# Kernel tuning notes

Hardware: AMD Instinct MI355X
Metric: run time of the kernel (lower is better)

Reference implementation:

```python
import jax, jax.numpy as jnp
import numpy as np

B, T, E, H = 8, 2048, 1024, 128

def setup_inputs() -> dict:
    key = jax.random.key(0)
    k1, k2, k3, k4 = jax.random.split(key, 4)
    s = 0.02
    return {
        "x":  jax.random.normal(k1, (B, T, E), dtype=jnp.float32),
        "Wq": jax.random.normal(k2, (E, H), dtype=jnp.float32) * s,
        "Wk": jax.random.normal(k3, (E, H), dtype=jnp.float32) * s,
        "Wv": jax.random.normal(k4, (E, H), dtype=jnp.float32) * s,
    }

def reference(x, Wq, Wk, Wv):
    # q,k,v: [B,T,H]
    q = jnp.einsum("bte,eh->bth", x, Wq)
    k = jnp.einsum("bte,eh->bth", x, Wk)
    v = jnp.einsum("bte,eh->bth", x, Wv)
    scale = jnp.asarray(q.shape[-1], q.dtype) ** -0.5
    wei = jnp.einsum("bqh,bkh->bqk", q, k) * scale  # [B,T,T]
    causal = jnp.tril(jnp.ones((wei.shape[1], wei.shape[2]), dtype=bool))
    wei = jnp.where(causal, wei, jnp.asarray(-jnp.inf, wei.dtype))
    wei = jax.nn.softmax(wei, axis=-1)
    # dropout_prob = 0.0 -> identity
    return jnp.einsum("bqk,bkh->bqh", wei, v)
```

## Files before the change

### kernel.cpp

```cpp
#include <hip/hip_runtime.h>

#define BB 8
#define TT 2048
#define EE 1024
#define HH 128

typedef __bf16 bf16;
typedef __attribute__((ext_vector_type(8))) __bf16 bf16x8;
typedef __attribute__((ext_vector_type(4))) __bf16 bf16x4;
typedef __attribute__((ext_vector_type(4))) float f32x4;
typedef __attribute__((ext_vector_type(16))) float f32x16;

__device__ __host__ inline int qb_off(int qb) {
  int h = qb >> 1;
  return qb + h * (h - 1) + ((qb & 1) ? h : 0);
}
#define NSLAB 72

__device__ inline void gload_lds16(const bf16* g, bf16* l) {
  __builtin_amdgcn_global_load_lds((const __attribute__((address_space(1))) unsigned int*)g,
                                   (__attribute__((address_space(3))) unsigned int*)l,
                                   16, 0, 0);
}

__global__ __launch_bounds__(256) void prep_kernel(const float* __restrict__ x,
                                                   bf16* __restrict__ xb,
                                                   const float* __restrict__ wq,
                                                   const float* __restrict__ wk,
                                                   const float* __restrict__ wv,
                                                   bf16* __restrict__ wt) {
  __shared__ float tile[64][65];
  const int bid = blockIdx.x;
  if (bid < 4096) {
    const size_t base = (size_t)bid * 4096 + threadIdx.x * 4;
#pragma unroll
    for (int j = 0; j < 4; ++j) {
      size_t idx = base + j * 1024;
      f32x4 xv = *(const f32x4*)(x + idx);
      bf16x4 xo;
#pragma unroll
      for (int i = 0; i < 4; ++i) xo[i] = (bf16)xv[i];
      *(bf16x4*)(xb + idx) = xo;
    }
  } else {
    const int id = bid - 4096;
    const int z = id >> 5;
    const int h0 = ((id >> 4) & 1) * 64;
    const int k0 = (id & 15) * 64;
    const float* w = (z == 0) ? wq : ((z == 1) ? wk : wv);
    const int c = threadIdx.x & 63;
    const int r0 = threadIdx.x >> 6;
#pragma unroll
    for (int i = 0; i < 16; ++i) {
      int tt = r0 + i * 4;
      tile[tt][c] = w[(size_t)(k0 + tt) * HH + h0 + c];
    }
    __syncthreads();
#pragma unroll
    for (int i = 0; i < 16; ++i) {
      int hh = r0 + i * 4;
      wt[((size_t)(z * HH + h0 + hh)) * EE + k0 + c] = (bf16)tile[c][hh];
    }
  }
}

__global__ __launch_bounds__(256) void gemm_kernel(const bf16* __restrict__ xb,
                                                   const bf16* __restrict__ wt,
                                                   bf16* __restrict__ q,
                                                   bf16* __restrict__ k,
                                                   bf16* __restrict__ vt) {
  __shared__ bf16 As[2][128 * 32];
  __shared__ bf16 Bs[2][96 * 32];
  const int tid = threadIdx.x;
  const int lane = tid & 63;
  const int wave = tid >> 6;
  const int l16 = lane & 15;
  const int quad = lane >> 4;
  const int wm = wave & 1;
  const int wn = wave >> 1;
  const int bm = blockIdx.x;
  const int ntile = blockIdx.y;

  const int trow = tid >> 2;
  const int tsub = (tid & 3) * 8;
  const bf16* gA = xb + (size_t)(bm * 128 + trow) * EE + tsub;
  const bf16* gB = wt + (size_t)(ntile * 96 + trow) * EE + tsub;

  f32x4 acc[4][3];
#pragma unroll
  for (int rg = 0; rg < 4; ++rg)
#pragma unroll
    for (int nt = 0; nt < 3; ++nt) acc[rg][nt] = f32x4{0.f, 0.f, 0.f, 0.f};

  auto stage = [&](int bufi, int ks) {
    gload_lds16(gA + ks * 32, &As[bufi][wave * 512]);
    gload_lds16(gA + (size_t)64 * EE + ks * 32, &As[bufi][2048 + wave * 512]);
    gload_lds16(gB + ks * 32, &Bs[bufi][wave * 512]);
    if (tid < 128)
      gload_lds16(gB + (size_t)64 * EE + ks * 32, &Bs[bufi][2048 + wave * 512]);
  };

  stage(0, 0);
  __syncthreads();

  int buf = 0;
  for (int ks = 0; ks < EE / 32; ++ks) {
    if (ks < EE / 32 - 1) stage(buf ^ 1, ks + 1);

    bf16x8 af[4], bf_[3];
#pragma unroll
    for (int rg = 0; rg < 4; ++rg)
      af[rg] = *(const bf16x8*)&As[buf][(wm * 64 + rg * 16 + l16) * 32 + quad * 8];
#pragma unroll
    for (int nt = 0; nt < 3; ++nt)
      bf_[nt] = *(const bf16x8*)&Bs[buf][(wn * 48 + nt * 16 + l16) * 32 + quad * 8];
#pragma unroll
    for (int rg = 0; rg < 4; ++rg)
#pragma unroll
      for (int nt = 0; nt < 3; ++nt)
        acc[rg][nt] = __builtin_amdgcn_mfma_f32_16x16x32_bf16(af[rg], bf_[nt], acc[rg][nt], 0, 0, 0);

    __syncthreads();
    buf ^= 1;
  }

#pragma unroll
  for (int rg = 0; rg < 4; ++rg)
#pragma unroll
    for (int nt = 0; nt < 3; ++nt) {
      int col = ntile * 96 + wn * 48 + nt * 16 + l16;
      int z = col >> 7;
      int n = col & 127;
      int row0 = bm * 128 + wm * 64 + rg * 16 + quad * 4;
      if (z == 2) {
        int bb = row0 >> 11;
        int t0 = row0 & (TT - 1);
        bf16x4 pkv;
#pragma unroll
        for (int r = 0; r < 4; ++r) pkv[r] = (bf16)acc[rg][nt][r];
        *(bf16x4*)&vt[((size_t)(bb * HH + n)) * TT + t0] = pkv;
      } else {
        bf16* op = (z == 0) ? q : k;
#pragma unroll
        for (int r = 0; r < 4; ++r)
          op[(size_t)(row0 + r) * HH + n] = (bf16)acc[rg][nt][r];
      }
    }
}

__device__ __forceinline__ unsigned pk2(float a, float b) {
  union { __bf16 h[2]; unsigned u; } x;
  x.h[0] = (__bf16)a;
  x.h[1] = (__bf16)b;
  return x.u;
}

__device__ __forceinline__ void plswap(unsigned& a, unsigned& b) {
  asm volatile("v_permlane32_swap_b32 %0, %1" : "+v"(a), "+v"(b));
}

__global__ __launch_bounds__(256, 2) void flash_kernel(const bf16* __restrict__ q,
                                                       const bf16* __restrict__ k,
                                                       const bf16* __restrict__ vt,
                                                       bf16* __restrict__ opart,
                                                       float* __restrict__ lpart) {
  __shared__ bf16 Ks[2][64 * 128];
  __shared__ bf16 Vs[128 * 64];

  const int b = blockIdx.x & 7;
  int j = (NSLAB - 1) - (blockIdx.x >> 3);
  int qb = 0, ns = 1;
  while (j >= ns) { j -= ns; ++qb; ns = ((2 * qb + 1) >> 2) + 1; }
  const int s = j;
  const int kt0 = s * 4;
  const int kt1 = min(kt0 + 3, 2 * qb + 1);

  const int tid = threadIdx.x;
  const int lane = tid & 63;
  const int wave = tid >> 6;
  const int l32 = lane & 31;
  const int hi = lane >> 5;
  const int qrow = qb * 128 + wave * 32 + l32;
  const int kdiag = qb * 4 + wave;

  bf16x8 qf[8];
  {
    const bf16* qp = q + (size_t)(b * TT + qrow) * HH + hi * 8;
#pragma unroll
    for (int h16 = 0; h16 < 8; ++h16) qf[h16] = *(const bf16x8*)(qp + h16 * 16);
  }

  f32x16 O[4];
#pragma unroll
  for (int ht = 0; ht < 4; ++ht)
#pragma unroll
    for (int r = 0; r < 16; ++r) O[ht][r] = 0.f;
  float L = 0.f;

  const int krow_s = tid >> 4;
  const int kchk_s = (tid & 15) ^ (krow_s & 7);
  const int vrow_s = tid >> 3;
  const int vchk_s = (tid & 7) ^ (vrow_s & 7);
  const bf16* kg = k + (size_t)b * TT * HH;
  const bf16* vg = vt + (size_t)b * HH * TT;

  auto stageK = [&](int bufi, int kt) {
#pragma unroll
    for (int i = 0; i < 4; ++i)
      gload_lds16(kg + (size_t)(kt * 64 + i * 16 + krow_s) * HH + kchk_s * 8,
                  &Ks[bufi][(i * 256 + wave * 64) * 8]);
  };
  auto stageV = [&](int kt) {
#pragma unroll
    for (int i = 0; i < 4; ++i)
      gload_lds16(vg + (size_t)(i * 32 + vrow_s) * TT + kt * 64 + vchk_s * 8,
                  &Vs[(i * 256 + wave * 64) * 8]);
  };

  const int kxor = (l32 & 7) << 3;
  const float c_ = 0.12753257680406733f;

  stageK(0, kt0);
  stageV(kt0);
  __syncthreads();

  int buf = 0;
  for (int kt = kt0; kt <= kt1; ++kt) {
    if (kt < kt1) stageK(buf ^ 1, kt + 1);

#pragma unroll
    for (int khalf = 0; khalf < 2; ++khalf) {
      const int k32 = kt * 2 + khalf;
      if (k32 <= kdiag) {
        const bf16* kls = &Ks[buf][(khalf * 32 + l32) * 128];
        bf16x8 kf[8];
#pragma unroll
        for (int h16 = 0; h16 < 8; ++h16)
          kf[h16] = *(const bf16x8*)&kls[(h16 * 16 + hi * 8) ^ kxor];

        f32x16 S;
#pragma unroll
        for (int r = 0; r < 16; ++r) S[r] = 0.f;
        __builtin_amdgcn_s_setprio(1);
#pragma unroll
        for (int h16 = 0; h16 < 8; ++h16)
          S = __builtin_amdgcn_mfma_f32_32x32x16_bf16(kf[h16], qf[h16], S, 0, 0, 0);
        __builtin_amdgcn_s_setprio(0);

        float p[16];
        if (k32 == kdiag) {
          const int kkb = k32 * 32 + 4 * hi;
#pragma unroll
          for (int r = 0; r < 16; ++r) {
            int kk = kkb + (r & 3) + 8 * (r >> 2);
            p[r] = (kk <= qrow) ? exp2f(S[r] * c_) : 0.f;
          }
        } else {
#pragma unroll
          for (int r = 0; r < 16; ++r) p[r] = exp2f(S[r] * c_);
        }
        L += (((p[0] + p[1]) + (p[2] + p[3])) + ((p[4] + p[5]) + (p[6] + p[7]))) +
             (((p[8] + p[9]) + (p[10] + p[11])) + ((p[12] + p[13]) + (p[14] + p[15])));

#pragma unroll
        for (int s16 = 0; s16 < 2; ++s16) {
          unsigned w0 = pk2(p[s16 * 8 + 0], p[s16 * 8 + 1]);
          unsigned w1 = pk2(p[s16 * 8 + 2], p[s16 * 8 + 3]);
          unsigned w2 = pk2(p[s16 * 8 + 4], p[s16 * 8 + 5]);
          unsigned w3 = pk2(p[s16 * 8 + 6], p[s16 * 8 + 7]);
          plswap(w0, w2);
          plswap(w1, w3);
          union { unsigned u[4]; bf16x8 v; } af;
          af.u[0] = w0;
          af.u[1] = w1;
          af.u[2] = w2;
          af.u[3] = w3;
          bf16x8 vf[4];
#pragma unroll
          for (int ht = 0; ht < 4; ++ht)
            vf[ht] = *(const bf16x8*)&Vs[(l32 + 32 * ht) * 64 +
                                         ((khalf * 32 + s16 * 16 + hi * 8) ^ kxor)];
          __builtin_amdgcn_s_setprio(1);
#pragma unroll
          for (int ht = 0; ht < 4; ++ht)
            O[ht] = __builtin_amdgcn_mfma_f32_32x32x16_bf16(af.v, vf[ht], O[ht], 0, 0, 0);
          __builtin_amdgcn_s_setprio(0);
        }
      }
    }
    __syncthreads();
    if (kt < kt1) {
      stageV(kt + 1);
      __syncthreads();
    }
    buf ^= 1;
  }

  L += __shfl_xor(L, 32, 64);

  const size_t slab = (size_t)(b * NSLAB + qb_off(qb) + s);
  bf16* op = opart + slab * (128 * 128) + (size_t)wave * 32 * 128;
#pragma unroll
  for (int ht = 0; ht < 4; ++ht)
#pragma unroll
    for (int r = 0; r < 16; ++r) {
      int qr = (r & 3) + 8 * (r >> 2) + 4 * hi;
      op[qr * 128 + ht * 32 + l32] = (bf16)O[ht][r];
    }
  if (hi == 0) lpart[slab * 128 + wave * 32 + l32] = L;
}

__global__ __launch_bounds__(128) void combine_kernel(const bf16* __restrict__ opart,
                                                      const float* __restrict__ lpart,
                                                      float* __restrict__ out) {
  const int b = blockIdx.x;
  const int qt16 = blockIdx.y;
  const int half = blockIdx.z;
  const int row = threadIdx.x >> 3;
  const int colo = (threadIdx.x & 7) * 8 + half * 64;
  const int qb = qt16 >> 3;
  const int srow = (qt16 & 7) * 16 + row;
  const int ns = ((2 * qb + 1) >> 2) + 1;
  const size_t slab0 = (size_t)(b * NSLAB + qb_off(qb));

  float acc[8];
#pragma unroll
  for (int j = 0; j < 8; ++j) acc[j] = 0.f;
  float L = 0.f;

  int s = 0;
  for (; s + 4 <= ns; s += 4) {
    float l0 = lpart[(slab0 + s + 0) * 128 + srow];
    float l1 = lpart[(slab0 + s + 1) * 128 + srow];
    float l2 = lpart[(slab0 + s + 2) * 128 + srow];
    float l3 = lpart[(slab0 + s + 3) * 128 + srow];
    bf16x8 v0 = *(const bf16x8*)(opart + (slab0 + s + 0) * (128 * 128) + srow * 128 + colo);
    bf16x8 v1 = *(const bf16x8*)(opart + (slab0 + s + 1) * (128 * 128) + srow * 128 + colo);
    bf16x8 v2 = *(const bf16x8*)(opart + (slab0 + s + 2) * (128 * 128) + srow * 128 + colo);
    bf16x8 v3 = *(const bf16x8*)(opart + (slab0 + s + 3) * (128 * 128) + srow * 128 + colo);
    L += (l0 + l1) + (l2 + l3);
#pragma unroll
    for (int j = 0; j < 8; ++j)
      acc[j] += ((float)v0[j] + (float)v1[j]) + ((float)v2[j] + (float)v3[j]);
  }
  for (; s < ns; ++s) {
    L += lpart[(slab0 + s) * 128 + srow];
    bf16x8 ov = *(const bf16x8*)(opart + (slab0 + s) * (128 * 128) + srow * 128 + colo);
#pragma unroll
    for (int j = 0; j < 8; ++j) acc[j] += (float)ov[j];
  }
  float invL = 1.f / L;
  float* o = out + ((size_t)(b * TT + qt16 * 16 + row)) * HH + colo;
  f32x4 o0, o1;
#pragma unroll
  for (int j = 0; j < 4; ++j) { o0[j] = acc[j] * invL; o1[j] = acc[j + 4] * invL; }
  *(f32x4*)o = o0;
  *(f32x4*)(o + 4) = o1;
}

extern "C" void kernel_launch(void* const* d_in, const int* in_sizes, int n_in,
                              void* d_out, int out_size, void* d_ws, size_t ws_size,
                              hipStream_t stream) {
  const float* x = (const float*)d_in[0];
  const float* wq = (const float*)d_in[1];
  const float* wk = (const float*)d_in[2];
  const float* wv = (const float*)d_in[3];
  float* out = (float*)d_out;

  char* ws = (char*)d_ws;
  const size_t NE = (size_t)BB * TT * HH;
  bf16* wt = (bf16*)ws;
  bf16* xb = (bf16*)(ws + (1 << 20));
  bf16* q = (bf16*)(ws + (33 << 20));
  bf16* k = q + NE;
  bf16* vt = k + NE;
  bf16* opart = xb;
  float* lpart = (float*)(opart + (size_t)(BB * NSLAB) * 128 * 128);

  prep_kernel<<<dim3(4192), 256, 0, stream>>>(x, xb, wq, wk, wv, wt);
  gemm_kernel<<<dim3(128, 4), 256, 0, stream>>>(xb, wt, q, k, vt);
  flash_kernel<<<dim3(576), 256, 0, stream>>>(q, k, vt, opart, lpart);
  combine_kernel<<<dim3(8, 128, 2), 128, 0, stream>>>(opart, lpart, out);
}
```

Before: 153.9 us.

## Fuse fp32-to-bf16 conversion of x into the projection GEMM A-tile loads

The separate prep pass that converted all of x to a bf16 workspace copy is removed. The GEMM now reads fp32 x directly into registers, converts it to bf16, and writes it into the LDS A buffer with software prefetch one k-step ahead. The weight transpose stays in its own small kernel, and the workspace layout is compacted. This drops a full read and write pass over x, but each x tile is now read in fp32 by four column-tile blocks, and the A operand no longer uses async global-to-LDS loads, which raises register use and the cost of the GEMM main loop.

```diff
diff --git a/kernel.cpp b/kernel.cpp
--- a/kernel.cpp
+++ b/kernel.cpp
@@ -23,48 +23,31 @@
                                    16, 0, 0);
 }
 
-__global__ __launch_bounds__(256) void prep_kernel(const float* __restrict__ x,
-                                                   bf16* __restrict__ xb,
-                                                   const float* __restrict__ wq,
-                                                   const float* __restrict__ wk,
-                                                   const float* __restrict__ wv,
-                                                   bf16* __restrict__ wt) {
+__global__ __launch_bounds__(256) void wt_kernel(const float* __restrict__ wq,
+                                                 const float* __restrict__ wk,
+                                                 const float* __restrict__ wv,
+                                                 bf16* __restrict__ wt) {
   __shared__ float tile[64][65];
-  const int bid = blockIdx.x;
-  if (bid < 4096) {
-    const size_t base = (size_t)bid * 4096 + threadIdx.x * 4;
-#pragma unroll
-    for (int j = 0; j < 4; ++j) {
-      size_t idx = base + j * 1024;
-      f32x4 xv = *(const f32x4*)(x + idx);
-      bf16x4 xo;
-#pragma unroll
-      for (int i = 0; i < 4; ++i) xo[i] = (bf16)xv[i];
-      *(bf16x4*)(xb + idx) = xo;
-    }
-  } else {
-    const int id = bid - 4096;
-    const int z = id >> 5;
-    const int h0 = ((id >> 4) & 1) * 64;
-    const int k0 = (id & 15) * 64;
-    const float* w = (z == 0) ? wq : ((z == 1) ? wk : wv);
-    const int c = threadIdx.x & 63;
-    const int r0 = threadIdx.x >> 6;
-#pragma unroll
-    for (int i = 0; i < 16; ++i) {
-      int tt = r0 + i * 4;
-      tile[tt][c] = w[(size_t)(k0 + tt) * HH + h0 + c];
-    }
-    __syncthreads();
-#pragma unroll
-    for (int i = 0; i < 16; ++i) {
-      int hh = r0 + i * 4;
-      wt[((size_t)(z * HH + h0 + hh)) * EE + k0 + c] = (bf16)tile[c][hh];
-    }
-  }
-}
-
-__global__ __launch_bounds__(256) void gemm_kernel(const bf16* __restrict__ xb,
+  const int z = blockIdx.z;
+  const float* w = (z == 0) ? wq : ((z == 1) ? wk : wv);
+  const int k0 = blockIdx.x * 64;
+  const int h0 = blockIdx.y * 64;
+  const int c = threadIdx.x & 63;
+  const int r0 = threadIdx.x >> 6;
+#pragma unroll
+  for (int i = 0; i < 16; ++i) {
+    int tt = r0 + i * 4;
+    tile[tt][c] = w[(size_t)(k0 + tt) * HH + h0 + c];
+  }
+  __syncthreads();
+#pragma unroll
+  for (int i = 0; i < 16; ++i) {
+    int hh = r0 + i * 4;
+    wt[((size_t)(z * HH + h0 + hh)) * EE + k0 + c] = (bf16)tile[c][hh];
+  }
+}
+
+__global__ __launch_bounds__(256) void gemm_kernel(const float* __restrict__ x,
                                                    const bf16* __restrict__ wt,
                                                    bf16* __restrict__ q,
                                                    bf16* __restrict__ k,
@@ -83,8 +66,9 @@
 
   const int trow = tid >> 2;
   const int tsub = (tid & 3) * 8;
-  const bf16* gA = xb + (size_t)(bm * 128 + trow) * EE + tsub;
+  const float* gA = x + (size_t)(bm * 128 + trow) * EE + tsub;
   const bf16* gB = wt + (size_t)(ntile * 96 + trow) * EE + tsub;
+  const int awr = trow * 32 + tsub;
 
   f32x4 acc[4][3];
 #pragma unroll
@@ -92,21 +76,31 @@
 #pragma unroll
     for (int nt = 0; nt < 3; ++nt) acc[rg][nt] = f32x4{0.f, 0.f, 0.f, 0.f};
 
-  auto stage = [&](int bufi, int ks) {
-    gload_lds16(gA + ks * 32, &As[bufi][wave * 512]);
-    gload_lds16(gA + (size_t)64 * EE + ks * 32, &As[bufi][2048 + wave * 512]);
+  auto stageB = [&](int bufi, int ks) {
     gload_lds16(gB + ks * 32, &Bs[bufi][wave * 512]);
     if (tid < 128)
       gload_lds16(gB + (size_t)64 * EE + ks * 32, &Bs[bufi][2048 + wave * 512]);
   };
-
-  stage(0, 0);
+  auto packA = [](f32x4 a0, f32x4 a1) {
+    bf16x8 ab;
+#pragma unroll
+    for (int jj = 0; jj < 4; ++jj) { ab[jj] = (bf16)a0[jj]; ab[jj + 4] = (bf16)a1[jj]; }
+    return ab;
+  };
+
+  {
+    f32x4 a0 = *(const f32x4*)(gA);
+    f32x4 a1 = *(const f32x4*)(gA + 4);
+    f32x4 a2 = *(const f32x4*)(gA + (size_t)64 * EE);
+    f32x4 a3 = *(const f32x4*)(gA + (size_t)64 * EE + 4);
+    stageB(0, 0);
+    *(bf16x8*)&As[0][awr] = packA(a0, a1);
+    *(bf16x8*)&As[0][2048 + awr] = packA(a2, a3);
+  }
   __syncthreads();
 
   int buf = 0;
   for (int ks = 0; ks < EE / 32; ++ks) {
-    if (ks < EE / 32 - 1) stage(buf ^ 1, ks + 1);
-
     bf16x8 af[4], bf_[3];
 #pragma unroll
     for (int rg = 0; rg < 4; ++rg)
@@ -114,12 +108,27 @@
 #pragma unroll
     for (int nt = 0; nt < 3; ++nt)
       bf_[nt] = *(const bf16x8*)&Bs[buf][(wn * 48 + nt * 16 + l16) * 32 + quad * 8];
+
+    f32x4 a0, a1, a2, a3;
+    if (ks < EE / 32 - 1) {
+      const float* gn = gA + (ks + 1) * 32;
+      a0 = *(const f32x4*)(gn);
+      a1 = *(const f32x4*)(gn + 4);
+      a2 = *(const f32x4*)(gn + (size_t)64 * EE);
+      a3 = *(const f32x4*)(gn + (size_t)64 * EE + 4);
+      stageB(buf ^ 1, ks + 1);
+    }
+
 #pragma unroll
     for (int rg = 0; rg < 4; ++rg)
 #pragma unroll
       for (int nt = 0; nt < 3; ++nt)
         acc[rg][nt] = __builtin_amdgcn_mfma_f32_16x16x32_bf16(af[rg], bf_[nt], acc[rg][nt], 0, 0, 0);
 
+    if (ks < EE / 32 - 1) {
+      *(bf16x8*)&As[buf ^ 1][awr] = packA(a0, a1);
+      *(bf16x8*)&As[buf ^ 1][2048 + awr] = packA(a2, a3);
+    }
     __syncthreads();
     buf ^= 1;
   }
@@ -370,15 +379,14 @@
   char* ws = (char*)d_ws;
   const size_t NE = (size_t)BB * TT * HH;
   bf16* wt = (bf16*)ws;
-  bf16* xb = (bf16*)(ws + (1 << 20));
-  bf16* q = (bf16*)(ws + (33 << 20));
+  bf16* q = (bf16*)(ws + (1 << 20));
   bf16* k = q + NE;
   bf16* vt = k + NE;
-  bf16* opart = xb;
+  bf16* opart = (bf16*)(ws + (16 << 20));
   float* lpart = (float*)(opart + (size_t)(BB * NSLAB) * 128 * 128);
 
-  prep_kernel<<<dim3(4192), 256, 0, stream>>>(x, xb, wq, wk, wv, wt);
-  gemm_kernel<<<dim3(128, 4), 256, 0, stream>>>(xb, wt, q, k, vt);
+  wt_kernel<<<dim3(16, 2, 3), 256, 0, stream>>>(wq, wk, wv, wt);
+  gemm_kernel<<<dim3(128, 4), 256, 0, stream>>>(x, wt, q, k, vt);
   flash_kernel<<<dim3(576), 256, 0, stream>>>(q, k, vt, opart, lpart);
   combine_kernel<<<dim3(8, 128, 2), 128, 0, stream>>>(opart, lpart, out);
 }
```

Result: slower. 160.4 us (+4.3%).
